# Kernel tuning notes

Measured on AMD Instinct MI355X. Metric: run time of the kernel, lower is better.

The kernel has to match this reference:

```python
import jax, jax.numpy as jnp
from jax import lax
import numpy as np

D_MODEL = 768
D_STATE = 64
D_CONV = 4
EXPAND = 2
HEADDIM = 128
NGROUPS = 1
D_INNER = EXPAND * D_MODEL            # 1536
NHEADS = D_INNER // HEADDIM           # 12
D_IN_PROJ = 2 * D_INNER + 2 * NGROUPS * D_STATE + NHEADS  # 3212
CONV_DIM = D_INNER + 2 * NGROUPS * D_STATE                # 1664
BATCH, SEQLEN = 2, 4096
EPS = 1e-5


def setup_inputs() -> dict:
    key = jax.random.key(0)
    ks = jax.random.split(key, 8)
    u = jax.random.normal(ks[0], (BATCH, SEQLEN, D_MODEL), jnp.float32)
    W_in = jax.random.normal(ks[1], (D_IN_PROJ, D_MODEL), jnp.float32) * 0.02
    conv_w = jax.random.normal(ks[2], (CONV_DIM, D_CONV), jnp.float32) * 0.2
    conv_b = jnp.zeros((CONV_DIM,), jnp.float32)
    # dt_bias init as in BaseMambaBlock: inv-softplus of dt ~ logU(dt_min, dt_max)
    dt = jnp.exp(jax.random.uniform(ks[3], (NHEADS,)) * (np.log(0.1) - np.log(0.001)) + np.log(0.001))
    dt = jnp.clip(dt, 1e-4, None)
    dt_bias = dt + jnp.log(-jnp.expm1(-dt))
    A_log = jnp.log(jnp.abs(jax.random.normal(ks[4], (NHEADS,), jnp.float32)))
    Dp = jnp.ones((NHEADS,), jnp.float32)
    norm_w = jnp.ones((D_INNER,), jnp.float32)
    W_out = jax.random.normal(ks[5], (D_MODEL, D_INNER), jnp.float32) * 0.02
    return dict(u=u, W_in=W_in, conv_w=conv_w, conv_b=conv_b, dt_bias=dt_bias,
                A_log=A_log, Dp=Dp, norm_w=norm_w, W_out=W_out)


def _silu(x):
    return x * jax.nn.sigmoid(x)


def _depthwise_causal_conv(x, w, b):
    # x: [B, L, C], w: [C, W], b: [C]. Causal: left-pad W-1, crop to L.
    Bt, L, C = x.shape
    xp = jnp.pad(x, ((0, 0), (D_CONV - 1, 0), (0, 0)))
    # stack D_CONV shifted views: [B, L, C, W]
    taps = jnp.stack([xp[:, k:k + L, :] for k in range(D_CONV)], axis=-1)
    return jnp.einsum('blcw,cw->blc', taps, w) + b


def reference(u, W_in, conv_w, conv_b, dt_bias, A_log, Dp, norm_w, W_out):
    Bt, L, _ = u.shape
    zxbcdt = jnp.einsum('bld,ed->ble', u, W_in)  # [B, L, 3212]
    z = zxbcdt[..., :D_INNER]                                   # [B,L,1536]
    xBC = zxbcdt[..., D_INNER:D_INNER + CONV_DIM]               # [B,L,1664]
    dt = zxbcdt[..., D_INNER + CONV_DIM:]                       # [B,L,H]
    dt = jax.nn.softplus(dt + dt_bias)                          # [B,L,H]

    xBC = _silu(_depthwise_causal_conv(xBC, conv_w, conv_b))
    x = xBC[..., :D_INNER].reshape(Bt, L, NHEADS, HEADDIM)      # [B,L,H,P]
    Bm = xBC[..., D_INNER:D_INNER + NGROUPS * D_STATE]          # [B,L,N] (ngroups=1)
    Cm = xBC[..., D_INNER + NGROUPS * D_STATE:]                 # [B,L,N]

    A = -jnp.exp(A_log)                                         # [H]
    dA = jnp.exp(dt * A)                                        # [B,L,H]

    # time-major scan over the selective-state-space recurrence
    xs = (jnp.swapaxes(x, 0, 1),   # [L,B,H,P]
          jnp.swapaxes(dt, 0, 1),  # [L,B,H]
          jnp.swapaxes(dA, 0, 1),  # [L,B,H]
          jnp.swapaxes(Bm, 0, 1),  # [L,B,N]
          jnp.swapaxes(Cm, 0, 1))  # [L,B,N]

    def step(state, inp):
        x_t, dt_t, dA_t, B_t, C_t = inp
        # state: [B,H,P,N]
        state = state * dA_t[..., None, None] + (dt_t[..., None] * x_t)[..., None] * B_t[:, None, None, :]
        y_t = jnp.einsum('bhpn,bn->bhp', state, C_t)
        return state, y_t

    state0 = jnp.zeros((Bt, NHEADS, HEADDIM, D_STATE), u.dtype)
    _, y = lax.scan(step, state0, xs)                           # y: [L,B,H,P]
    y = jnp.swapaxes(y, 0, 1) + Dp[None, None, :, None] * x     # skip term D*x
    y = y.reshape(Bt, L, D_INNER)

    # RMSNormGated, norm_before_gate=False: normalize(y * silu(z)) * weight
    g = y * _silu(z)
    g = g * jax.lax.rsqrt(jnp.mean(g * g, axis=-1, keepdims=True) + EPS) * norm_w
    return jnp.einsum('bli,di->bld', g, W_out)
```

## Files before the change

### kernel.cpp

```cpp
#include <hip/hip_runtime.h>
#include <hip/hip_bf16.h>
#include <stdint.h>

#define BATCH   2
#define SEQLEN  4096
#define DMODEL  768
#define DSTATE  64
#define DCONV   4
#define HEADDIM 128
#define NHEADS  12
#define DINNER  1536
#define DINPROJ 3212
#define CONVDIM 1664
#define DXBC    1676
#define NPAD1   3328
#define ROWS    (BATCH*SEQLEN)
#define CHUNK   64
#define NCHUNK  (SEQLEN/CHUNK)
#define CROWS   8
#define TBUF    4096

typedef __bf16 bf16x8 __attribute__((ext_vector_type(8)));
typedef float  f32x4  __attribute__((ext_vector_type(4)));

__device__ __forceinline__ f32x4 splat4(float v) { return (f32x4){v, v, v, v}; }

__device__ __forceinline__ void load_lds16(const void* g, void* l) {
    __builtin_amdgcn_global_load_lds(
        (const __attribute__((address_space(1))) unsigned int*)g,
        (__attribute__((address_space(3))) unsigned int*)l, 16, 0, 0);
}

__global__ void cvt_bf16_kernel(const float* __restrict__ src,
                                __hip_bfloat16* __restrict__ dst, int n) {
    int i = (blockIdx.x * blockDim.x + threadIdx.x) * 4;
    if (i + 3 < n) {
        float4 v = *(const float4*)(src + i);
        dst[i + 0] = __float2bfloat16(v.x);
        dst[i + 1] = __float2bfloat16(v.y);
        dst[i + 2] = __float2bfloat16(v.z);
        dst[i + 3] = __float2bfloat16(v.w);
    } else {
        for (; i < n; ++i) dst[i] = __float2bfloat16(src[i]);
    }
}

__global__ void padw1_kernel(const float* __restrict__ src,
                             __hip_bfloat16* __restrict__ dst) {
    int i = blockIdx.x * blockDim.x + threadIdx.x;
    if (i >= NPAD1 * DMODEL) return;
    int r = i / DMODEL;
    float v = (r < DINPROJ) ? src[i] : 0.f;
    dst[i] = __float2bfloat16(v);
}

__global__ __launch_bounds__(256) void gemm_bf16_nt(
    const __hip_bfloat16* __restrict__ A,
    const __hip_bfloat16* __restrict__ Bt,
    float* __restrict__ C,
    int M, int Nreal, int K, int ldc)
{
    __shared__ __align__(16) __hip_bfloat16 As[2 * TBUF];
    __shared__ __align__(16) __hip_bfloat16 Bs[2 * TBUF];
    const int tid  = threadIdx.x;
    const int lane = tid & 63;
    const int wave = tid >> 6;
    const int wm   = wave >> 1;
    const int wn   = wave & 1;
    const int tm   = blockIdx.x * 128;
    const int tn   = blockIdx.y * 128;

    f32x4 acc[4][4] = {};

    const int lrow = tid >> 2;
    const int lk8s = ((tid & 3) * 8) ^ (((tid >> 3) & 3) << 3);
    const __hip_bfloat16* gA0 = A  + (size_t)(tm + lrow)      * K + lk8s;
    const __hip_bfloat16* gA1 = A  + (size_t)(tm + lrow + 64) * K + lk8s;
    const __hip_bfloat16* gB0 = Bt + (size_t)(tn + lrow)      * K + lk8s;
    const __hip_bfloat16* gB1 = Bt + (size_t)(tn + lrow + 64) * K + lk8s;

    const int fr  = lane & 15;
    const int fks = ((lane >> 4) * 8) ^ (((lane >> 1) & 3) << 3);

    load_lds16(gA0, As + tid * 8);
    load_lds16(gA1, As + tid * 8 + 2048);
    load_lds16(gB0, Bs + tid * 8);
    load_lds16(gB1, Bs + tid * 8 + 2048);
    __syncthreads();

    int bufo = 0;
    for (int kk = 0; kk < K; kk += 32) {
        const int nbufo = bufo ^ TBUF;
        if (kk + 32 < K) {
            load_lds16(gA0 + kk + 32, As + nbufo + tid * 8);
            load_lds16(gA1 + kk + 32, As + nbufo + tid * 8 + 2048);
            load_lds16(gB0 + kk + 32, Bs + nbufo + tid * 8);
            load_lds16(gB1 + kk + 32, Bs + nbufo + tid * 8 + 2048);
        }
        bf16x8 af[4], bfr[4];
#pragma unroll
        for (int i = 0; i < 4; ++i) {
            af[i]  = *(const bf16x8*)(As + bufo + (wm * 64 + i * 16 + fr) * 32 + fks);
            bfr[i] = *(const bf16x8*)(Bs + bufo + (wn * 64 + i * 16 + fr) * 32 + fks);
        }
#pragma unroll
        for (int mi = 0; mi < 4; ++mi)
#pragma unroll
            for (int ni = 0; ni < 4; ++ni)
                acc[mi][ni] = __builtin_amdgcn_mfma_f32_16x16x32_bf16(
                    af[mi], bfr[ni], acc[mi][ni], 0, 0, 0);
        __syncthreads();
        bufo = nbufo;
    }

    const int rq = (lane >> 4) * 4;
#pragma unroll
    for (int mi = 0; mi < 4; ++mi) {
#pragma unroll
        for (int ni = 0; ni < 4; ++ni) {
            int col = tn + wn * 64 + ni * 16 + fr;
            if (col < Nreal) {
                size_t rbase = (size_t)(tm + wm * 64 + mi * 16 + rq) * ldc + col;
#pragma unroll
                for (int j = 0; j < 4; ++j)
                    C[rbase + (size_t)j * ldc] = acc[mi][ni][j];
            }
        }
    }
}

__global__ __launch_bounds__(256) void gemm1_fused(
    const __hip_bfloat16* __restrict__ A,
    const __hip_bfloat16* __restrict__ Bt,
    float* __restrict__ Cz,
    float* __restrict__ Cx)
{
    __shared__ __align__(16) __hip_bfloat16 As[2 * TBUF];
    __shared__ __align__(16) __hip_bfloat16 Bs[2 * TBUF];
    const int tid  = threadIdx.x;
    const int lane = tid & 63;
    const int wave = tid >> 6;
    const int wm   = wave >> 1;
    const int wn   = wave & 1;
    const int tm   = blockIdx.x * 128;
    const int tn   = blockIdx.y * 128;
    const int K    = DMODEL;

    float* Co;
    int ldc2, cb, nb;
    if (tn < DINNER) { Co = Cz; ldc2 = DINNER; cb = tn;          nb = DINNER; }
    else             { Co = Cx; ldc2 = DXBC;   cb = tn - DINNER; nb = DXBC;   }

    f32x4 acc[4][4] = {};

    const int lrow = tid >> 2;
    const int lk8s = ((tid & 3) * 8) ^ (((tid >> 3) & 3) << 3);
    const __hip_bfloat16* gA0 = A  + (size_t)(tm + lrow)      * K + lk8s;
    const __hip_bfloat16* gA1 = A  + (size_t)(tm + lrow + 64) * K + lk8s;
    const __hip_bfloat16* gB0 = Bt + (size_t)(tn + lrow)      * K + lk8s;
    const __hip_bfloat16* gB1 = Bt + (size_t)(tn + lrow + 64) * K + lk8s;

    const int fr  = lane & 15;
    const int fks = ((lane >> 4) * 8) ^ (((lane >> 1) & 3) << 3);

    load_lds16(gA0, As + tid * 8);
    load_lds16(gA1, As + tid * 8 + 2048);
    load_lds16(gB0, Bs + tid * 8);
    load_lds16(gB1, Bs + tid * 8 + 2048);
    __syncthreads();

    int bufo = 0;
    for (int kk = 0; kk < K; kk += 32) {
        const int nbufo = bufo ^ TBUF;
        if (kk + 32 < K) {
            load_lds16(gA0 + kk + 32, As + nbufo + tid * 8);
            load_lds16(gA1 + kk + 32, As + nbufo + tid * 8 + 2048);
            load_lds16(gB0 + kk + 32, Bs + nbufo + tid * 8);
            load_lds16(gB1 + kk + 32, Bs + nbufo + tid * 8 + 2048);
        }
        bf16x8 af[4], bfr[4];
#pragma unroll
        for (int i = 0; i < 4; ++i) {
            af[i]  = *(const bf16x8*)(As + bufo + (wm * 64 + i * 16 + fr) * 32 + fks);
            bfr[i] = *(const bf16x8*)(Bs + bufo + (wn * 64 + i * 16 + fr) * 32 + fks);
        }
#pragma unroll
        for (int mi = 0; mi < 4; ++mi)
#pragma unroll
            for (int ni = 0; ni < 4; ++ni)
                acc[mi][ni] = __builtin_amdgcn_mfma_f32_16x16x32_bf16(
                    af[mi], bfr[ni], acc[mi][ni], 0, 0, 0);
        __syncthreads();
        bufo = nbufo;
    }

    const int rq = (lane >> 4) * 4;
#pragma unroll
    for (int mi = 0; mi < 4; ++mi) {
#pragma unroll
        for (int ni = 0; ni < 4; ++ni) {
            int col = cb + wn * 64 + ni * 16 + fr;
            if (col < nb) {
                size_t rbase = (size_t)(tm + wm * 64 + mi * 16 + rq) * ldc2 + col;
#pragma unroll
                for (int j = 0; j < 4; ++j)
                    Co[rbase + (size_t)j * ldc2] = acc[mi][ni][j];
            }
        }
    }
}

__global__ void conv_kernel(const float* __restrict__ xbcdt,
                            const float* __restrict__ convw,
                            const float* __restrict__ convb,
                            const float* __restrict__ dt_bias,
                            const float* __restrict__ A_log,
                            float* __restrict__ xbuf,
                            float* __restrict__ Bm,
                            float* __restrict__ Cm,
                            float* __restrict__ dtb,
                            float* __restrict__ dAb)
{
    int c = blockIdx.x * 256 + threadIdx.x;
    size_t row0 = (size_t)blockIdx.y * CROWS;
    if (c < CONVDIM) {
        int l0 = (int)(row0 & (SEQLEN - 1));
        float w0 = convw[c * 4 + 0];
        float w1 = convw[c * 4 + 1];
        float w2 = convw[c * 4 + 2];
        float w3 = convw[c * 4 + 3];
        float bias = convb[c];
        const float* src = xbcdt + row0 * DXBC + c;
        float x0 = (l0 >= 3) ? src[-3 * DXBC] : 0.f;
        float x1 = (l0 >= 2) ? src[-2 * DXBC] : 0.f;
        float x2 = (l0 >= 1) ? src[-1 * DXBC] : 0.f;
#pragma unroll
        for (int r = 0; r < CROWS; ++r) {
            float x3 = src[(size_t)r * DXBC];
            float acc = bias + x0 * w0 + x1 * w1 + x2 * w2 + x3 * w3;
            float v = acc / (1.f + __expf(-acc));
            size_t row = row0 + r;
            if (c < DINNER)               xbuf[row * DINNER + c] = v;
            else if (c < DINNER + DSTATE) Bm[row * DSTATE + (c - DINNER)] = v;
            else                          Cm[row * DSTATE + (c - DINNER - DSTATE)] = v;
            x0 = x1; x1 = x2; x2 = x3;
        }
    } else if (c < DXBC) {
        int h = c - CONVDIM;
        float bias = dt_bias[h];
        float A = -__expf(A_log[h]);
        const float* src = xbcdt + row0 * DXBC + c;
#pragma unroll
        for (int r = 0; r < CROWS; ++r) {
            float v = src[(size_t)r * DXBC] + bias;
            float dt = (v > 20.f) ? v : log1pf(__expf(v));
            size_t row = row0 + r;
            dtb[row * NHEADS + h] = dt;
            dAb[row * NHEADS + h] = __expf(dt * A);
        }
    }
}

__global__ __launch_bounds__(256) void chunk_state_f32(
    const float* __restrict__ xbuf, const float* __restrict__ Bm,
    const float* __restrict__ dtb, const float* __restrict__ dAb,
    float* __restrict__ Sloc, float* __restrict__ Pk)
{
    const int blk = blockIdx.x;
    const int k   = blk % NCHUNK;
    const int bh  = blk / NCHUNK;
    const int h   = bh % NHEADS;
    const int b   = bh / NHEADS;
    const int tid = threadIdx.x;
    const int pg  = tid >> 3;
    const int n0  = (tid & 7) * 8;
    const size_t row0 = (size_t)b * SEQLEN + k * CHUNK;
    const float* xbase = xbuf + (row0 * NHEADS + h) * HEADDIM + pg * 4;

    __shared__ __align__(16) float lB[CHUNK][DSTATE];
    __shared__ float lDA[CHUNK];
    __shared__ float ldt[CHUNK];

    for (int i = tid; i < CHUNK * DSTATE / 4; i += 256)
        ((float4*)&lB[0][0])[i] = ((const float4*)(Bm + row0 * DSTATE))[i];
    if (tid < CHUNK) {
        lDA[tid] = dAb[(row0 + tid) * NHEADS + h];
        ldt[tid] = dtb[(row0 + tid) * NHEADS + h];
    }
    __syncthreads();

    f32x4 s4[4][2] = {};
    f32x4 xt0[4], xt1[4];

#pragma unroll
    for (int tt = 0; tt < 4; ++tt)
        xt0[tt] = *(const f32x4*)(xbase + (size_t)tt * (NHEADS * HEADDIM));

#pragma unroll
    for (int tile = 0; tile < 16; ++tile) {
        f32x4* cur = (tile & 1) ? xt1 : xt0;
        f32x4* nxt = (tile & 1) ? xt0 : xt1;
        if (tile < 15) {
#pragma unroll
            for (int tt = 0; tt < 4; ++tt)
                nxt[tt] = *(const f32x4*)(xbase +
                    (size_t)((tile + 1) * 4 + tt) * (NHEADS * HEADDIM));
        }
#pragma unroll
        for (int tt = 0; tt < 4; ++tt) {
            int t = tile * 4 + tt;
            f32x4 da4 = splat4(lDA[t]);
            float dtv = ldt[t];
            f32x4 bv0 = *(const f32x4*)&lB[t][n0];
            f32x4 bv1 = *(const f32x4*)&lB[t][n0 + 4];
#pragma unroll
            for (int pl = 0; pl < 4; ++pl) {
                f32x4 dtx = splat4(dtv * cur[tt][pl]);
                s4[pl][0] = s4[pl][0] * da4 + dtx * bv0;
                s4[pl][1] = s4[pl][1] * da4 + dtx * bv1;
            }
        }
    }

    const size_t kbase = (size_t)(bh * NCHUNK + k) * (HEADDIM * DSTATE);
#pragma unroll
    for (int pl = 0; pl < 4; ++pl) {
        size_t a = kbase + (size_t)(pg * 4 + pl) * DSTATE + n0;
        *(f32x4*)(Sloc + a)     = s4[pl][0];
        *(f32x4*)(Sloc + a + 4) = s4[pl][1];
    }

    if (tid == 0) {
        float pr = 1.f;
#pragma unroll 8
        for (int t = 0; t < CHUNK; ++t) pr *= lDA[t];
        Pk[bh * NCHUNK + k] = pr;
    }
}

__global__ __launch_bounds__(256) void scan_phase2(
    float* __restrict__ Sloc, const float* __restrict__ Pk)
{
    int bh = blockIdx.x >> 5;
    int eo = (blockIdx.x & 31) * 256 + threadIdx.x;
    __shared__ float lP[NCHUNK];
    if (threadIdx.x < NCHUNK) lP[threadIdx.x] = Pk[bh * NCHUNK + threadIdx.x];
    __syncthreads();
    float s = 0.f;
    size_t base = (size_t)bh * NCHUNK * 8192 + eo;
#pragma unroll 8
    for (int k = 0; k < NCHUNK; ++k) {
        size_t a = base + (size_t)k * 8192;
        float f = Sloc[a];
        Sloc[a] = s;
        s = s * lP[k] + f;
    }
}

__global__ __launch_bounds__(256) void chunk_y_f32(
    const float* __restrict__ xbuf, const float* __restrict__ Bm,
    const float* __restrict__ Cm, const float* __restrict__ dtb,
    const float* __restrict__ dAb, const float* __restrict__ Dp,
    const float* __restrict__ Sini, float* __restrict__ ybuf)
{
    const int blk = blockIdx.x;
    const int k   = blk % NCHUNK;
    const int bh  = blk / NCHUNK;
    const int h   = bh % NHEADS;
    const int b   = bh / NHEADS;
    const int tid = threadIdx.x;
    const int pg  = tid >> 2;
    const int q   = tid & 3;
    const int n0  = q * 16;
    const size_t row0 = (size_t)b * SEQLEN + k * CHUNK;
    const float* xbase = xbuf + (row0 * NHEADS + h) * HEADDIM + pg * 2;
    float* ybase = ybuf + (row0 * NHEADS + h) * HEADDIM + pg * 2;

    __shared__ __align__(16) float lB[CHUNK][DSTATE];
    __shared__ __align__(16) float lC[CHUNK][DSTATE];
    __shared__ float lDA[CHUNK];
    __shared__ float ldt[CHUNK];

    for (int i = tid; i < CHUNK * DSTATE / 4; i += 256) {
        ((float4*)&lB[0][0])[i] = ((const float4*)(Bm + row0 * DSTATE))[i];
        ((float4*)&lC[0][0])[i] = ((const float4*)(Cm + row0 * DSTATE))[i];
    }
    if (tid < CHUNK) {
        lDA[tid] = dAb[(row0 + tid) * NHEADS + h];
        ldt[tid] = dtb[(row0 + tid) * NHEADS + h];
    }

    f32x4 s4[2][4];
    const size_t kbase = (size_t)(bh * NCHUNK + k) * (HEADDIM * DSTATE);
#pragma unroll
    for (int pl = 0; pl < 2; ++pl) {
        size_t a = kbase + (size_t)(pg * 2 + pl) * DSTATE + n0;
#pragma unroll
        for (int nq = 0; nq < 4; ++nq)
            s4[pl][nq] = *(const f32x4*)(Sini + a + nq * 4);
    }
    const float dph = Dp[h];

    float xa[2][8], xb[2][8];
#pragma unroll
    for (int tt = 0; tt < 8; ++tt) {
        float2 v = *(const float2*)(xbase + (size_t)tt * (NHEADS * HEADDIM));
        xa[0][tt] = v.x; xa[1][tt] = v.y;
    }
    __syncthreads();

#pragma unroll
    for (int tile = 0; tile < 8; ++tile) {
        float (*cur)[8] = (tile & 1) ? xb : xa;
        float (*nxt)[8] = (tile & 1) ? xa : xb;
        if (tile < 7) {
#pragma unroll
            for (int tt = 0; tt < 8; ++tt) {
                float2 v = *(const float2*)(xbase +
                    (size_t)((tile + 1) * 8 + tt) * (NHEADS * HEADDIM));
                nxt[0][tt] = v.x; nxt[1][tt] = v.y;
            }
        }
#pragma unroll
        for (int tt = 0; tt < 8; ++tt) {
            int t = tile * 8 + tt;
            f32x4 da4 = splat4(lDA[t]);
            float dtv = ldt[t];
            f32x4 bv0 = *(const f32x4*)&lB[t][n0];
            f32x4 bv1 = *(const f32x4*)&lB[t][n0 + 4];
            f32x4 bv2 = *(const f32x4*)&lB[t][n0 + 8];
            f32x4 bv3 = *(const f32x4*)&lB[t][n0 + 12];
            f32x4 cv0 = *(const f32x4*)&lC[t][n0];
            f32x4 cv1 = *(const f32x4*)&lC[t][n0 + 4];
            f32x4 cv2 = *(const f32x4*)&lC[t][n0 + 8];
            f32x4 cv3 = *(const f32x4*)&lC[t][n0 + 12];
            float yr[2];
#pragma unroll
            for (int pl = 0; pl < 2; ++pl) {
                f32x4 dtx = splat4(dtv * cur[pl][tt]);
                f32x4 v0 = s4[pl][0] * da4 + dtx * bv0;
                f32x4 v1 = s4[pl][1] * da4 + dtx * bv1;
                f32x4 v2 = s4[pl][2] * da4 + dtx * bv2;
                f32x4 v3 = s4[pl][3] * da4 + dtx * bv3;
                s4[pl][0] = v0; s4[pl][1] = v1; s4[pl][2] = v2; s4[pl][3] = v3;
                f32x4 y4 = cv0 * v0 + cv1 * v1 + cv2 * v2 + cv3 * v3;
                float y = (y4[0] + y4[1]) + (y4[2] + y4[3]);
                y += __shfl_xor(y, 1);
                y += __shfl_xor(y, 2);
                yr[pl] = y;
            }
            if (q == 0) {
                float2 w = {yr[0] + dph * cur[0][tt], yr[1] + dph * cur[1][tt]};
                *(float2*)(ybase + (size_t)t * (NHEADS * HEADDIM)) = w;
            }
        }
    }
}

#define NT 64
__global__ __launch_bounds__(256) void scan_kernel(
    const float* __restrict__ xbuf, const float* __restrict__ Bm,
    const float* __restrict__ Cm, const float* __restrict__ dtb,
    const float* __restrict__ dAb, const float* __restrict__ Dp,
    float* __restrict__ ybuf)
{
    int blk = blockIdx.x;
    int ps = blk & 7;
    int h  = (blk >> 3) % NHEADS;
    int b  = blk / (NHEADS * 8);
    int p0 = ps * 16;
    int tid = threadIdx.x;
    int pl  = tid >> 4;
    int n0  = (tid & 15) * 4;

    __shared__ __align__(16) float lB[NT][64];
    __shared__ __align__(16) float lC[NT][64];
    __shared__ __align__(16) float lDtx[NT][16];
    __shared__ float lDA[NT];
    __shared__ float lY[NT][16];

    float s0 = 0.f, s1 = 0.f, s2 = 0.f, s3 = 0.f;
    float dph = Dp[h];
    size_t rowbase = (size_t)b * SEQLEN;

    for (int t0 = 0; t0 < SEQLEN; t0 += NT) {
        for (int i = tid; i < NT * 64 / 4; i += 256) {
            ((float4*)&lB[0][0])[i] = ((const float4*)Bm)[(rowbase + t0) * 16 + i];
            ((float4*)&lC[0][0])[i] = ((const float4*)Cm)[(rowbase + t0) * 16 + i];
        }
        for (int i = tid; i < NT * 16; i += 256) {
            int t = i >> 4, pp = i & 15;
            size_t r = rowbase + t0 + t;
            lDtx[t][pp] = dtb[r * NHEADS + h] * xbuf[(r * NHEADS + h) * HEADDIM + p0 + pp];
        }
        if (tid < NT) lDA[tid] = dAb[(rowbase + t0 + tid) * NHEADS + h];
        __syncthreads();

        for (int t = 0; t < NT; ++t) {
            float da  = lDA[t];
            float dtx = lDtx[t][pl];
            const float* bp = &lB[t][n0];
            const float* cp = &lC[t][n0];
            s0 = s0 * da + dtx * bp[0];
            s1 = s1 * da + dtx * bp[1];
            s2 = s2 * da + dtx * bp[2];
            s3 = s3 * da + dtx * bp[3];
            float part = s0 * cp[0] + s1 * cp[1] + s2 * cp[2] + s3 * cp[3];
            part += __shfl_xor(part, 1);
            part += __shfl_xor(part, 2);
            part += __shfl_xor(part, 4);
            part += __shfl_xor(part, 8);
            if ((tid & 15) == 0) lY[t][pl] = part;
        }
        __syncthreads();

        for (int i = tid; i < NT * 16; i += 256) {
            int t = i >> 4, pp = i & 15;
            size_t r = rowbase + t0 + t;
            size_t gi = (r * NHEADS + h) * HEADDIM + p0 + pp;
            ybuf[gi] = lY[t][pp] + dph * xbuf[gi];
        }
        __syncthreads();
    }
}

__global__ __launch_bounds__(256) void gate_rms_kernel(
    const float* __restrict__ ybuf, const float* __restrict__ zbuf,
    const float* __restrict__ norm_w, __hip_bfloat16* __restrict__ gbf)
{
    int row = blockIdx.x;
    int tid = threadIdx.x;
    const float2* y2 = (const float2*)(ybuf + (size_t)row * DINNER);
    const float2* z2 = (const float2*)(zbuf + (size_t)row * DINNER);
    const float2* nw2 = (const float2*)norm_w;
    float g[6];
    float ss = 0.f;
#pragma unroll
    for (int j = 0; j < 3; ++j) {
        int idx = tid + j * 256;
        float2 yy = y2[idx];
        float2 zz = z2[idx];
        float g0 = yy.x * (zz.x / (1.f + __expf(-zz.x)));
        float g1 = yy.y * (zz.y / (1.f + __expf(-zz.y)));
        g[j * 2 + 0] = g0;
        g[j * 2 + 1] = g1;
        ss += g0 * g0 + g1 * g1;
    }
#pragma unroll
    for (int m = 1; m < 64; m <<= 1) ss += __shfl_xor(ss, m);
    __shared__ float red[4];
    if ((tid & 63) == 0) red[tid >> 6] = ss;
    __syncthreads();
    float tot = red[0] + red[1] + red[2] + red[3];
    float scale = rsqrtf(tot * (1.f / DINNER) + 1e-5f);
#pragma unroll
    for (int j = 0; j < 3; ++j) {
        int idx = tid + j * 256;
        float2 w = nw2[idx];
        __hip_bfloat162 o;
        o.x = __float2bfloat16(g[j * 2 + 0] * scale * w.x);
        o.y = __float2bfloat16(g[j * 2 + 1] * scale * w.y);
        *(__hip_bfloat162*)(gbf + (size_t)row * DINNER + idx * 2) = o;
    }
}

extern "C" void kernel_launch(void* const* d_in, const int* in_sizes, int n_in,
                              void* d_out, int out_size, void* d_ws, size_t ws_size,
                              hipStream_t stream)
{
    const float* u       = (const float*)d_in[0];
    const float* W_in    = (const float*)d_in[1];
    const float* conv_w  = (const float*)d_in[2];
    const float* conv_b  = (const float*)d_in[3];
    const float* dt_bias = (const float*)d_in[4];
    const float* A_log   = (const float*)d_in[5];
    const float* Dp      = (const float*)d_in[6];
    const float* norm_w  = (const float*)d_in[7];
    const float* W_out   = (const float*)d_in[8];
    float* out = (float*)d_out;

    char* ws = (char*)d_ws;
    size_t off = 0;
    auto alloc = [&](size_t bytes) {
        char* p = ws + off;
        off += (bytes + 255) & ~(size_t)255;
        return p;
    };
    __hip_bfloat16* ubf  = (__hip_bfloat16*)alloc((size_t)ROWS * DMODEL * 2);
    __hip_bfloat16* W1bf = (__hip_bfloat16*)alloc((size_t)NPAD1 * DMODEL * 2);
    __hip_bfloat16* W2bf = (__hip_bfloat16*)alloc((size_t)DMODEL * DINNER * 2);
    float* zbuf  = (float*)alloc((size_t)ROWS * DINNER * 4);
    float* xbcdt = (float*)alloc((size_t)ROWS * DXBC * 4);
    float* xbuf = (float*)alloc((size_t)ROWS * DINNER * 4);
    float* Bmb  = (float*)alloc((size_t)ROWS * DSTATE * 4);
    float* Cmb  = (float*)alloc((size_t)ROWS * DSTATE * 4);
    float* dtb  = (float*)alloc((size_t)ROWS * NHEADS * 4);
    float* dAb  = (float*)alloc((size_t)ROWS * NHEADS * 4);
    float* ybuf = (float*)alloc((size_t)ROWS * DINNER * 4);
    float* Pkb  = (float*)alloc((size_t)BATCH * NHEADS * NCHUNK * 4);
    __hip_bfloat16* gbf = (__hip_bfloat16*)xbuf;
    float* Sloc = (float*)xbcdt;
    bool chunked = (off <= ws_size);

    cvt_bf16_kernel<<<(ROWS * DMODEL / 4 + 255) / 256, 256, 0, stream>>>(u, ubf, ROWS * DMODEL);
    padw1_kernel<<<(NPAD1 * DMODEL + 255) / 256, 256, 0, stream>>>(W_in, W1bf);
    cvt_bf16_kernel<<<(DMODEL * DINNER / 4 + 255) / 256, 256, 0, stream>>>(W_out, W2bf, DMODEL * DINNER);

    gemm1_fused<<<dim3(ROWS / 128, NPAD1 / 128), 256, 0, stream>>>(
        ubf, W1bf, zbuf, xbcdt);

    conv_kernel<<<dim3((DXBC + 255) / 256, ROWS / CROWS), 256, 0, stream>>>(
        xbcdt, conv_w, conv_b, dt_bias, A_log, xbuf, Bmb, Cmb, dtb, dAb);

    if (chunked) {
        chunk_state_f32<<<BATCH * NHEADS * NCHUNK, 256, 0, stream>>>(
            xbuf, Bmb, dtb, dAb, Sloc, Pkb);
        scan_phase2<<<BATCH * NHEADS * 32, 256, 0, stream>>>(Sloc, Pkb);
        chunk_y_f32<<<BATCH * NHEADS * NCHUNK, 256, 0, stream>>>(
            xbuf, Bmb, Cmb, dtb, dAb, Dp, Sloc, ybuf);
    } else {
        scan_kernel<<<BATCH * NHEADS * 8, 256, 0, stream>>>(
            xbuf, Bmb, Cmb, dtb, dAb, Dp, ybuf);
    }

    gate_rms_kernel<<<ROWS, 256, 0, stream>>>(ybuf, zbuf, norm_w, gbf);

    gemm_bf16_nt<<<dim3(ROWS / 128, DMODEL / 128), 256, 0, stream>>>(
        gbf, W2bf, out, ROWS, DMODEL, DINNER, DMODEL);
}
```

Measured before the change: 296.1 us.

## Store chunk states in bf16 and merge weight/input conversion into one kernel

Chunk-local SSM states written by chunk_state, rescanned by scan_phase2 and read by chunk_y are now stored as bf16 instead of fp32, halving that intermediate traffic. The running prefix in scan_phase2 stays in fp32. The three fp32-to-bf16 conversion launches for u, W_in (padded) and W_out are merged into one prep kernel, saving two launches and vectorizing the W_in padding pass. Rounding the inter-chunk states to bf16 adds precision loss in the recurrence.

```diff
diff --git a/kernel.cpp b/kernel.cpp
--- a/kernel.cpp
+++ b/kernel.cpp
@@ -22,8 +22,17 @@
 
 typedef __bf16 bf16x8 __attribute__((ext_vector_type(8)));
 typedef float  f32x4  __attribute__((ext_vector_type(4)));
+typedef unsigned short u16x8 __attribute__((ext_vector_type(8)));
 
 __device__ __forceinline__ f32x4 splat4(float v) { return (f32x4){v, v, v, v}; }
+
+__device__ __forceinline__ unsigned short f2bf(float f) {
+    __hip_bfloat16 h = __float2bfloat16(f);
+    return *reinterpret_cast<unsigned short*>(&h);
+}
+__device__ __forceinline__ float bf2f(unsigned short u) {
+    return __uint_as_float(((unsigned int)u) << 16);
+}
 
 __device__ __forceinline__ void load_lds16(const void* g, void* l) {
     __builtin_amdgcn_global_load_lds(
@@ -31,27 +40,44 @@
         (__attribute__((address_space(3))) unsigned int*)l, 16, 0, 0);
 }
 
-__global__ void cvt_bf16_kernel(const float* __restrict__ src,
-                                __hip_bfloat16* __restrict__ dst, int n) {
-    int i = (blockIdx.x * blockDim.x + threadIdx.x) * 4;
-    if (i + 3 < n) {
-        float4 v = *(const float4*)(src + i);
-        dst[i + 0] = __float2bfloat16(v.x);
-        dst[i + 1] = __float2bfloat16(v.y);
-        dst[i + 2] = __float2bfloat16(v.z);
-        dst[i + 3] = __float2bfloat16(v.w);
-    } else {
-        for (; i < n; ++i) dst[i] = __float2bfloat16(src[i]);
-    }
-}
-
-__global__ void padw1_kernel(const float* __restrict__ src,
-                             __hip_bfloat16* __restrict__ dst) {
-    int i = blockIdx.x * blockDim.x + threadIdx.x;
-    if (i >= NPAD1 * DMODEL) return;
-    int r = i / DMODEL;
-    float v = (r < DINPROJ) ? src[i] : 0.f;
-    dst[i] = __float2bfloat16(v);
+#define NPREP1 (ROWS*DMODEL)
+#define NPREP2 (NPAD1*DMODEL)
+#define NPREP3 (DMODEL*DINNER)
+__global__ void prep_kernel(const float* __restrict__ u,
+                            const float* __restrict__ W_in,
+                            const float* __restrict__ W_out,
+                            __hip_bfloat16* __restrict__ ubf,
+                            __hip_bfloat16* __restrict__ W1bf,
+                            __hip_bfloat16* __restrict__ W2bf)
+{
+    int i = (blockIdx.x * 256 + threadIdx.x) * 4;
+    if (i < NPREP1) {
+        float4 v = *(const float4*)(u + i);
+        ubf[i + 0] = __float2bfloat16(v.x);
+        ubf[i + 1] = __float2bfloat16(v.y);
+        ubf[i + 2] = __float2bfloat16(v.z);
+        ubf[i + 3] = __float2bfloat16(v.w);
+    } else if (i < NPREP1 + NPREP2) {
+        int j = i - NPREP1;
+        int r = j / DMODEL;
+        if (r < DINPROJ) {
+            float4 v = *(const float4*)(W_in + j);
+            W1bf[j + 0] = __float2bfloat16(v.x);
+            W1bf[j + 1] = __float2bfloat16(v.y);
+            W1bf[j + 2] = __float2bfloat16(v.z);
+            W1bf[j + 3] = __float2bfloat16(v.w);
+        } else {
+            __hip_bfloat16 z = __float2bfloat16(0.f);
+            W1bf[j + 0] = z; W1bf[j + 1] = z; W1bf[j + 2] = z; W1bf[j + 3] = z;
+        }
+    } else if (i < NPREP1 + NPREP2 + NPREP3) {
+        int j = i - NPREP1 - NPREP2;
+        float4 v = *(const float4*)(W_out + j);
+        W2bf[j + 0] = __float2bfloat16(v.x);
+        W2bf[j + 1] = __float2bfloat16(v.y);
+        W2bf[j + 2] = __float2bfloat16(v.z);
+        W2bf[j + 3] = __float2bfloat16(v.w);
+    }
 }
 
 __global__ __launch_bounds__(256) void gemm_bf16_nt(
@@ -264,7 +290,7 @@
 __global__ __launch_bounds__(256) void chunk_state_f32(
     const float* __restrict__ xbuf, const float* __restrict__ Bm,
     const float* __restrict__ dtb, const float* __restrict__ dAb,
-    float* __restrict__ Sloc, float* __restrict__ Pk)
+    unsigned short* __restrict__ Sloc, float* __restrict__ Pk)
 {
     const int blk = blockIdx.x;
     const int k   = blk % NCHUNK;
@@ -326,8 +352,13 @@
 #pragma unroll
     for (int pl = 0; pl < 4; ++pl) {
         size_t a = kbase + (size_t)(pg * 4 + pl) * DSTATE + n0;
-        *(f32x4*)(Sloc + a)     = s4[pl][0];
-        *(f32x4*)(Sloc + a + 4) = s4[pl][1];
+        u16x8 o;
+#pragma unroll
+        for (int j = 0; j < 4; ++j) {
+            o[j]     = f2bf(s4[pl][0][j]);
+            o[4 + j] = f2bf(s4[pl][1][j]);
+        }
+        *(u16x8*)(Sloc + a) = o;
     }
 
     if (tid == 0) {
@@ -339,7 +370,7 @@
 }
 
 __global__ __launch_bounds__(256) void scan_phase2(
-    float* __restrict__ Sloc, const float* __restrict__ Pk)
+    unsigned short* __restrict__ Sloc, const float* __restrict__ Pk)
 {
     int bh = blockIdx.x >> 5;
     int eo = (blockIdx.x & 31) * 256 + threadIdx.x;
@@ -351,8 +382,8 @@
 #pragma unroll 8
     for (int k = 0; k < NCHUNK; ++k) {
         size_t a = base + (size_t)k * 8192;
-        float f = Sloc[a];
-        Sloc[a] = s;
+        float f = bf2f(Sloc[a]);
+        Sloc[a] = f2bf(s);
         s = s * lP[k] + f;
     }
 }
@@ -361,7 +392,7 @@
     const float* __restrict__ xbuf, const float* __restrict__ Bm,
     const float* __restrict__ Cm, const float* __restrict__ dtb,
     const float* __restrict__ dAb, const float* __restrict__ Dp,
-    const float* __restrict__ Sini, float* __restrict__ ybuf)
+    const unsigned short* __restrict__ Sini, float* __restrict__ ybuf)
 {
     const int blk = blockIdx.x;
     const int k   = blk % NCHUNK;
@@ -395,9 +426,15 @@
 #pragma unroll
     for (int pl = 0; pl < 2; ++pl) {
         size_t a = kbase + (size_t)(pg * 2 + pl) * DSTATE + n0;
-#pragma unroll
-        for (int nq = 0; nq < 4; ++nq)
-            s4[pl][nq] = *(const f32x4*)(Sini + a + nq * 4);
+        u16x8 v0 = *(const u16x8*)(Sini + a);
+        u16x8 v1 = *(const u16x8*)(Sini + a + 8);
+#pragma unroll
+        for (int j = 0; j < 4; ++j) {
+            s4[pl][0][j] = bf2f(v0[j]);
+            s4[pl][1][j] = bf2f(v0[4 + j]);
+            s4[pl][2][j] = bf2f(v1[j]);
+            s4[pl][3][j] = bf2f(v1[4 + j]);
+        }
     }
     const float dph = Dp[h];
 
@@ -599,12 +636,14 @@
     float* ybuf = (float*)alloc((size_t)ROWS * DINNER * 4);
     float* Pkb  = (float*)alloc((size_t)BATCH * NHEADS * NCHUNK * 4);
     __hip_bfloat16* gbf = (__hip_bfloat16*)xbuf;
-    float* Sloc = (float*)xbcdt;
+    unsigned short* Sloc = (unsigned short*)xbcdt;
     bool chunked = (off <= ws_size);
 
-    cvt_bf16_kernel<<<(ROWS * DMODEL / 4 + 255) / 256, 256, 0, stream>>>(u, ubf, ROWS * DMODEL);
-    padw1_kernel<<<(NPAD1 * DMODEL + 255) / 256, 256, 0, stream>>>(W_in, W1bf);
-    cvt_bf16_kernel<<<(DMODEL * DINNER / 4 + 255) / 256, 256, 0, stream>>>(W_out, W2bf, DMODEL * DINNER);
+    {
+        int ntot = (NPREP1 + NPREP2 + NPREP3) / 4;
+        prep_kernel<<<(ntot + 255) / 256, 256, 0, stream>>>(
+            u, W_in, W_out, ubf, W1bf, W2bf);
+    }
 
     gemm1_fused<<<dim3(ROWS / 128, NPAD1 / 128), 256, 0, stream>>>(
         ubf, W1bf, zbuf, xbcdt);
```

After: 278.9 us. -5.8%, faster.
